# Optimization experiments

Hardware: AMD Instinct MI355X
Metric: run time of the kernel (lower is better)

The kernel has to match this reference:

```python
import jax, jax.numpy as jnp
import numpy as np

TWO_PI = 2.0 * np.pi

def ringify(x):
    # wrap values to [-pi, pi)
    return (x + np.pi) % TWO_PI - np.pi

def complex_mean(x, axes):
    # circular mean direction: atan2(sum sin, sum ringify(cos))
    dir_x = ringify(jnp.cos(x)).sum(axis=axes)
    dir_y = jnp.sin(x).sum(axis=axes)
    return jnp.arctan2(dir_y, dir_x)

def setup_inputs() -> dict:
    key = jax.random.key(0)
    k1, k2, k3, k4 = jax.random.split(key, 4)
    B = 4096
    return {
        "x": jax.random.normal(k1, (B, 1, 28, 28), dtype=jnp.float32),
        "conv1_w": jax.random.normal(k2, (4, 1, 2, 2), dtype=jnp.float32),
        "conv2_w": jax.random.normal(k3, (8, 4, 4, 4), dtype=jnp.float32),
        "ff_w": jax.random.normal(k4, (288, 10), dtype=jnp.float32),
    }

def reference(x, conv1_w, conv2_w, ff_w):
    B = x.shape[0]
    x = ringify(x).reshape(B, 1, 28, 28)

    # --- ring conv1: 2x2 kernel, stride 2 (non-overlapping patches) ---
    # [B,1,28,28] -> [B,14,14,1,2,2]  (matches unfold(2,2,2).unfold(3,2,2).permute)
    p1 = x.reshape(B, 1, 14, 2, 14, 2).transpose(0, 2, 4, 1, 3, 5)
    w1 = conv1_w.transpose(1, 2, 3, 0)            # [1,2,2,4]
    d1 = ringify(p1[..., None] - w1)              # [B,14,14,1,2,2,4]
    h1 = complex_mean(d1, (3, 4, 5))              # [B,14,14,4]

    # --- ring conv2: 4x4 kernel, stride 2 (overlapping patches) ---
    h1 = h1.transpose(0, 3, 1, 2)                 # [B,4,14,14]
    idx = (jnp.arange(6) * 2)[:, None] + jnp.arange(4)[None, :]  # [6,4] window rows/cols
    p2 = h1[:, :, idx, :][:, :, :, :, idx]        # [B,4,6,4,6,4]
    p2 = p2.transpose(0, 2, 4, 1, 3, 5)           # [B,6,6,4,4,4]
    w2 = conv2_w.transpose(1, 2, 3, 0)            # [4,4,4,8]
    d2 = ringify(p2[..., None] - w2)              # [B,6,6,4,4,4,8]
    h2 = complex_mean(d2, (3, 4, 5))              # [B,6,6,8]

    # --- ring feed-forward ---
    f = h2.reshape(B, 288)
    d3 = ringify(f[:, :, None] - ff_w)            # [B,288,10]
    out = complex_mean(d3, (1,))                  # [B,10]
    return jnp.sin(out)
```

## Files before the change

### kernel.cpp

```cpp
#include <hip/hip_runtime.h>
#include <math.h>

#define FFT_OFF 0
#define W2_OFF 2880
#define W1_OFF 3400

__global__ void precompute_trig(const float* __restrict__ w1,
                                const float* __restrict__ w2,
                                const float* __restrict__ ff,
                                float2* __restrict__ ws) {
    int idx = blockIdx.x * blockDim.x + threadIdx.x;
    if (idx < 2880) {
        int k = idx / 10, n = idx % 10;
        float s, c; sincosf(ff[idx], &s, &c);
        ws[FFT_OFF + n * 288 + k] = make_float2(c, s);
    } else if (idx < 3392) {
        int i = idx - 2880;
        int oc = i >> 6, e = i & 63;
        float s, c; sincosf(w2[i], &s, &c);
        ws[W2_OFF + (oc >> 1) * 130 + e * 2 + (oc & 1)] = make_float2(c, s);
    } else if (idx < 3408) {
        int i = idx - 3392;
        float s, c; sincosf(w1[i], &s, &c);
        ws[W1_OFF + i] = make_float2(c, s);
    }
}

__device__ __forceinline__ void conv1_pos(float2 r0, float2 r1,
                                          const float2* __restrict__ w1t,
                                          float2* __restrict__ sc1,
                                          int pi, int pj) {
    float sx[4], cx[4];
    __sincosf(r0.x, &sx[0], &cx[0]);
    __sincosf(r0.y, &sx[1], &cx[1]);
    __sincosf(r1.x, &sx[2], &cx[2]);
    __sincosf(r1.y, &sx[3], &cx[3]);
    #pragma unroll
    for (int oc = 0; oc < 4; oc++) {
        float4 wa = *(const float4*)(w1t + oc * 4);
        float4 wb = *(const float4*)(w1t + oc * 4 + 2);
        float Y = 0.f, X = 0.f;
        Y = fmaf(sx[0], wa.x, fmaf(-cx[0], wa.y, Y));
        X = fmaf(cx[0], wa.x, fmaf( sx[0], wa.y, X));
        Y = fmaf(sx[1], wa.z, fmaf(-cx[1], wa.w, Y));
        X = fmaf(cx[1], wa.z, fmaf( sx[1], wa.w, X));
        Y = fmaf(sx[2], wb.x, fmaf(-cx[2], wb.y, Y));
        X = fmaf(cx[2], wb.x, fmaf( sx[2], wb.y, X));
        Y = fmaf(sx[3], wb.z, fmaf(-cx[3], wb.w, Y));
        X = fmaf(cx[3], wb.z, fmaf( sx[3], wb.w, X));
        float inv = rsqrtf(fmaxf(fmaf(X, X, Y * Y), 1e-30f));
        sc1[oc * 252 + pi * 18 + pj] = make_float2(Y * inv, X * inv);
    }
}

__global__ __launch_bounds__(256, 4) void ringnn_kernel(
    const float* __restrict__ x,
    const float2* __restrict__ ws,
    float* __restrict__ out)
{
    __shared__ __align__(16) float2 trig2[520];
    __shared__ __align__(16) float2 sc1[2 * 1008];
    __shared__ __align__(16) float2 sc2[2 * 288];
    const int tid = threadIdx.x;
    const float2* __restrict__ fft = ws + FFT_OFF;
    const float2* __restrict__ w1t = ws + W1_OFF;
    const size_t img0 = (size_t)blockIdx.x * 2;

    const int im0 = (tid >= 196) ? 1 : 0;
    const int p0  = tid - im0 * 196;
    const int pi0 = p0 / 14, pj0 = p0 % 14;
    const float* xb0 = x + (img0 + im0) * 784;
    float2 a0 = *(const float2*)(xb0 + (2 * pi0) * 28 + 2 * pj0);
    float2 a1 = *(const float2*)(xb0 + (2 * pi0 + 1) * 28 + 2 * pj0);
    int pi1 = 0, pj1 = 0;
    float2 b0 = make_float2(0.f, 0.f), b1 = make_float2(0.f, 0.f);
    if (tid < 136) {
        int p = tid + 60;
        pi1 = p / 14; pj1 = p % 14;
        const float* xb1 = x + (img0 + 1) * 784;
        b0 = *(const float2*)(xb1 + (2 * pi1) * 28 + 2 * pj1);
        b1 = *(const float2*)(xb1 + (2 * pi1 + 1) * 28 + 2 * pj1);
    }

    for (int i = tid; i < 260; i += 256)
        ((float4*)trig2)[i] = ((const float4*)(ws + W2_OFF))[i];

    conv1_pos(a0, a1, w1t, sc1 + im0 * 1008, pi0, pj0);
    if (tid < 136) conv1_pos(b0, b1, w1t, sc1 + 1008, pi1, pj1);
    __syncthreads();

    if (tid < 192) {
        const int img = (tid >= 96) ? 1 : 0;
        int r = tid - img * 96;
        int oi = r >> 4, ojg = (r >> 3) & 1, ocp = (r >> 1) & 3, hf = r & 1;
        const float2* wbp = trig2 + ocp * 130;
        const float2* s1p = sc1 + img * 1008;
        float aY[3][2] = {{0.f,0.f},{0.f,0.f},{0.f,0.f}};
        float aX[3][2] = {{0.f,0.f},{0.f,0.f},{0.f,0.f}};
        #pragma unroll
        for (int ch = 0; ch < 4; ch++) {
            #pragma unroll
            for (int kk = 0; kk < 2; kk++) {
                int ki = hf * 2 + kk;
                int base = ch * 252 + (oi * 2 + ki) * 18 + ojg * 6;
                float4 f0 = *(const float4*)(s1p + base);
                float4 f1 = *(const float4*)(s1p + base + 2);
                float4 f2 = *(const float4*)(s1p + base + 4);
                float4 f3 = *(const float4*)(s1p + base + 6);
                float ss[8] = {f0.x,f0.z,f1.x,f1.z,f2.x,f2.z,f3.x,f3.z};
                float cc[8] = {f0.y,f0.w,f1.y,f1.w,f2.y,f2.w,f3.y,f3.w};
                int e0 = ch * 16 + ki * 4;
                #pragma unroll
                for (int kj = 0; kj < 4; kj++) {
                    float4 wv = *(const float4*)(wbp + (e0 + kj) * 2);
                    #pragma unroll
                    for (int ojl = 0; ojl < 3; ojl++) {
                        float s = ss[ojl * 2 + kj], c = cc[ojl * 2 + kj];
                        aY[ojl][0] = fmaf(s, wv.x, fmaf(-c, wv.y, aY[ojl][0]));
                        aX[ojl][0] = fmaf(c, wv.x, fmaf( s, wv.y, aX[ojl][0]));
                        aY[ojl][1] = fmaf(s, wv.z, fmaf(-c, wv.w, aY[ojl][1]));
                        aX[ojl][1] = fmaf(c, wv.z, fmaf( s, wv.w, aX[ojl][1]));
                    }
                }
            }
        }
        #pragma unroll
        for (int ojl = 0; ojl < 3; ojl++) {
            float y0 = aY[ojl][0]; y0 += __shfl_xor(y0, 1);
            float y1 = aY[ojl][1]; y1 += __shfl_xor(y1, 1);
            float x0 = aX[ojl][0]; x0 += __shfl_xor(x0, 1);
            float x1 = aX[ojl][1]; x1 += __shfl_xor(x1, 1);
            float Y = hf ? y1 : y0;
            float X = hf ? x1 : x0;
            float inv = rsqrtf(fmaxf(fmaf(X, X, Y * Y), 1e-30f));
            int p = oi * 6 + ojg * 3 + ojl;
            sc2[img * 288 + p * 8 + ocp * 2 + hf] = make_float2(Y * inv, X * inv);
        }
    }
    __syncthreads();

    #pragma unroll
    for (int rr = 0; rr < 3; rr++) {
        int t = tid + (rr << 8);
        if (t < 640) {
            int img = (t >= 320) ? 1 : 0;
            int idx = t - img * 320;
            int n = idx >> 5, s = idx & 31;
            const float2* wn = fft + n * 288;
            const float2* s2p = sc2 + img * 288;
            float Y = 0.f, X = 0.f;
            #pragma unroll
            for (int i = 0; i < 9; i++) {
                int k = i * 32 + s;
                float2 sc = s2p[k];
                float2 w = wn[k];
                Y = fmaf(sc.x, w.x, fmaf(-sc.y, w.y, Y));
                X = fmaf(sc.y, w.x, fmaf( sc.x, w.y, X));
            }
            #pragma unroll
            for (int off = 16; off > 0; off >>= 1) {
                Y += __shfl_down(Y, off, 32);
                X += __shfl_down(X, off, 32);
            }
            if (s == 0) {
                out[(img0 + img) * 10 + n] =
                    Y * rsqrtf(fmaxf(fmaf(X, X, Y * Y), 1e-30f));
            }
        }
    }
}

extern "C" void kernel_launch(void* const* d_in, const int* in_sizes, int n_in,
                              void* d_out, int out_size, void* d_ws, size_t ws_size,
                              hipStream_t stream) {
    const float* x  = (const float*)d_in[0];
    const float* w1 = (const float*)d_in[1];
    const float* w2 = (const float*)d_in[2];
    const float* ff = (const float*)d_in[3];
    float* out = (float*)d_out;
    const int B = in_sizes[0] / 784;

    float2* ws = (float2*)d_ws;
    precompute_trig<<<14, 256, 0, stream>>>(w1, w2, ff, ws);
    ringnn_kernel<<<B / 2, 256, 0, stream>>>(x, ws, out);
}
```

Baseline: 82.39 us.

## Process two image pairs per block with prefetch of second pair's input

Each block now handles four images as two sequential pairs, with the grid halved. The second pair's input pixels are loaded into registers before the feed-forward phase of the first pair, so global load latency overlaps compute. The shared conv2 weight load is also amortized over twice as many images. In exchange there are half as many blocks, so latency hiding across blocks is lower, and the extra live registers may add pressure.

Measured after the change: 82.10 us. No clear change (-0.3%).

```diff
diff --git a/kernel.cpp b/kernel.cpp
--- a/kernel.cpp
+++ b/kernel.cpp
@@ -64,110 +64,129 @@
     const int tid = threadIdx.x;
     const float2* __restrict__ fft = ws + FFT_OFF;
     const float2* __restrict__ w1t = ws + W1_OFF;
-    const size_t img0 = (size_t)blockIdx.x * 2;
+    const size_t imgBase = (size_t)blockIdx.x * 4;
 
     const int im0 = (tid >= 196) ? 1 : 0;
     const int p0  = tid - im0 * 196;
     const int pi0 = p0 / 14, pj0 = p0 % 14;
-    const float* xb0 = x + (img0 + im0) * 784;
-    float2 a0 = *(const float2*)(xb0 + (2 * pi0) * 28 + 2 * pj0);
-    float2 a1 = *(const float2*)(xb0 + (2 * pi0 + 1) * 28 + 2 * pj0);
-    int pi1 = 0, pj1 = 0;
-    float2 b0 = make_float2(0.f, 0.f), b1 = make_float2(0.f, 0.f);
-    if (tid < 136) {
-        int p = tid + 60;
-        pi1 = p / 14; pj1 = p % 14;
-        const float* xb1 = x + (img0 + 1) * 784;
-        b0 = *(const float2*)(xb1 + (2 * pi1) * 28 + 2 * pj1);
-        b1 = *(const float2*)(xb1 + (2 * pi1 + 1) * 28 + 2 * pj1);
-    }
-
+    const int pr1 = tid + 60;
+    const int pi1 = pr1 / 14, pj1 = pr1 % 14;
+
+    float2 a0, a1, b0 = make_float2(0.f, 0.f), b1 = make_float2(0.f, 0.f);
+
+    auto loadPair = [&](size_t pairImg) {
+        const float* xb0 = x + (pairImg + im0) * 784;
+        a0 = *(const float2*)(xb0 + (2 * pi0) * 28 + 2 * pj0);
+        a1 = *(const float2*)(xb0 + (2 * pi0 + 1) * 28 + 2 * pj0);
+        if (tid < 136) {
+            const float* xb1 = x + (pairImg + 1) * 784;
+            b0 = *(const float2*)(xb1 + (2 * pi1) * 28 + 2 * pj1);
+            b1 = *(const float2*)(xb1 + (2 * pi1 + 1) * 28 + 2 * pj1);
+        }
+    };
+
+    auto phase1 = [&]() {
+        conv1_pos(a0, a1, w1t, sc1 + im0 * 1008, pi0, pj0);
+        if (tid < 136) conv1_pos(b0, b1, w1t, sc1 + 1008, pi1, pj1);
+    };
+
+    auto phase2 = [&]() {
+        if (tid < 192) {
+            const int img = (tid >= 96) ? 1 : 0;
+            int r = tid - img * 96;
+            int oi = r >> 4, ojg = (r >> 3) & 1, ocp = (r >> 1) & 3, hf = r & 1;
+            const float2* wbp = trig2 + ocp * 130;
+            const float2* s1p = sc1 + img * 1008;
+            float aY[3][2] = {{0.f,0.f},{0.f,0.f},{0.f,0.f}};
+            float aX[3][2] = {{0.f,0.f},{0.f,0.f},{0.f,0.f}};
+            #pragma unroll
+            for (int ch = 0; ch < 4; ch++) {
+                #pragma unroll
+                for (int kk = 0; kk < 2; kk++) {
+                    int ki = hf * 2 + kk;
+                    int base = ch * 252 + (oi * 2 + ki) * 18 + ojg * 6;
+                    float4 f0 = *(const float4*)(s1p + base);
+                    float4 f1 = *(const float4*)(s1p + base + 2);
+                    float4 f2 = *(const float4*)(s1p + base + 4);
+                    float4 f3 = *(const float4*)(s1p + base + 6);
+                    float ss[8] = {f0.x,f0.z,f1.x,f1.z,f2.x,f2.z,f3.x,f3.z};
+                    float cc[8] = {f0.y,f0.w,f1.y,f1.w,f2.y,f2.w,f3.y,f3.w};
+                    int e0 = ch * 16 + ki * 4;
+                    #pragma unroll
+                    for (int kj = 0; kj < 4; kj++) {
+                        float4 wv = *(const float4*)(wbp + (e0 + kj) * 2);
+                        #pragma unroll
+                        for (int ojl = 0; ojl < 3; ojl++) {
+                            float s = ss[ojl * 2 + kj], c = cc[ojl * 2 + kj];
+                            aY[ojl][0] = fmaf(s, wv.x, fmaf(-c, wv.y, aY[ojl][0]));
+                            aX[ojl][0] = fmaf(c, wv.x, fmaf( s, wv.y, aX[ojl][0]));
+                            aY[ojl][1] = fmaf(s, wv.z, fmaf(-c, wv.w, aY[ojl][1]));
+                            aX[ojl][1] = fmaf(c, wv.z, fmaf( s, wv.w, aX[ojl][1]));
+                        }
+                    }
+                }
+            }
+            #pragma unroll
+            for (int ojl = 0; ojl < 3; ojl++) {
+                float y0 = aY[ojl][0]; y0 += __shfl_xor(y0, 1);
+                float y1 = aY[ojl][1]; y1 += __shfl_xor(y1, 1);
+                float x0 = aX[ojl][0]; x0 += __shfl_xor(x0, 1);
+                float x1 = aX[ojl][1]; x1 += __shfl_xor(x1, 1);
+                float Y = hf ? y1 : y0;
+                float X = hf ? x1 : x0;
+                float inv = rsqrtf(fmaxf(fmaf(X, X, Y * Y), 1e-30f));
+                int p = oi * 6 + ojg * 3 + ojl;
+                sc2[img * 288 + p * 8 + ocp * 2 + hf] = make_float2(Y * inv, X * inv);
+            }
+        }
+    };
+
+    auto phase3 = [&](size_t pairImg) {
+        #pragma unroll
+        for (int rr = 0; rr < 3; rr++) {
+            int t = tid + (rr << 8);
+            if (t < 640) {
+                int img = (t >= 320) ? 1 : 0;
+                int idx = t - img * 320;
+                int n = idx >> 5, s = idx & 31;
+                const float2* wn = fft + n * 288;
+                const float2* s2p = sc2 + img * 288;
+                float Y = 0.f, X = 0.f;
+                #pragma unroll
+                for (int i = 0; i < 9; i++) {
+                    int k = i * 32 + s;
+                    float2 sc = s2p[k];
+                    float2 w = wn[k];
+                    Y = fmaf(sc.x, w.x, fmaf(-sc.y, w.y, Y));
+                    X = fmaf(sc.y, w.x, fmaf( sc.x, w.y, X));
+                }
+                #pragma unroll
+                for (int off = 16; off > 0; off >>= 1) {
+                    Y += __shfl_down(Y, off, 32);
+                    X += __shfl_down(X, off, 32);
+                }
+                if (s == 0) {
+                    out[(pairImg + img) * 10 + n] =
+                        Y * rsqrtf(fmaxf(fmaf(X, X, Y * Y), 1e-30f));
+                }
+            }
+        }
+    };
+
+    loadPair(imgBase);
     for (int i = tid; i < 260; i += 256)
         ((float4*)trig2)[i] = ((const float4*)(ws + W2_OFF))[i];
-
-    conv1_pos(a0, a1, w1t, sc1 + im0 * 1008, pi0, pj0);
-    if (tid < 136) conv1_pos(b0, b1, w1t, sc1 + 1008, pi1, pj1);
-    __syncthreads();
-
-    if (tid < 192) {
-        const int img = (tid >= 96) ? 1 : 0;
-        int r = tid - img * 96;
-        int oi = r >> 4, ojg = (r >> 3) & 1, ocp = (r >> 1) & 3, hf = r & 1;
-        const float2* wbp = trig2 + ocp * 130;
-        const float2* s1p = sc1 + img * 1008;
-        float aY[3][2] = {{0.f,0.f},{0.f,0.f},{0.f,0.f}};
-        float aX[3][2] = {{0.f,0.f},{0.f,0.f},{0.f,0.f}};
-        #pragma unroll
-        for (int ch = 0; ch < 4; ch++) {
-            #pragma unroll
-            for (int kk = 0; kk < 2; kk++) {
-                int ki = hf * 2 + kk;
-                int base = ch * 252 + (oi * 2 + ki) * 18 + ojg * 6;
-                float4 f0 = *(const float4*)(s1p + base);
-                float4 f1 = *(const float4*)(s1p + base + 2);
-                float4 f2 = *(const float4*)(s1p + base + 4);
-                float4 f3 = *(const float4*)(s1p + base + 6);
-                float ss[8] = {f0.x,f0.z,f1.x,f1.z,f2.x,f2.z,f3.x,f3.z};
-                float cc[8] = {f0.y,f0.w,f1.y,f1.w,f2.y,f2.w,f3.y,f3.w};
-                int e0 = ch * 16 + ki * 4;
-                #pragma unroll
-                for (int kj = 0; kj < 4; kj++) {
-                    float4 wv = *(const float4*)(wbp + (e0 + kj) * 2);
-                    #pragma unroll
-                    for (int ojl = 0; ojl < 3; ojl++) {
-                        float s = ss[ojl * 2 + kj], c = cc[ojl * 2 + kj];
-                        aY[ojl][0] = fmaf(s, wv.x, fmaf(-c, wv.y, aY[ojl][0]));
-                        aX[ojl][0] = fmaf(c, wv.x, fmaf( s, wv.y, aX[ojl][0]));
-                        aY[ojl][1] = fmaf(s, wv.z, fmaf(-c, wv.w, aY[ojl][1]));
-                        aX[ojl][1] = fmaf(c, wv.z, fmaf( s, wv.w, aX[ojl][1]));
-                    }
-                }
-            }
-        }
-        #pragma unroll
-        for (int ojl = 0; ojl < 3; ojl++) {
-            float y0 = aY[ojl][0]; y0 += __shfl_xor(y0, 1);
-            float y1 = aY[ojl][1]; y1 += __shfl_xor(y1, 1);
-            float x0 = aX[ojl][0]; x0 += __shfl_xor(x0, 1);
-            float x1 = aX[ojl][1]; x1 += __shfl_xor(x1, 1);
-            float Y = hf ? y1 : y0;
-            float X = hf ? x1 : x0;
-            float inv = rsqrtf(fmaxf(fmaf(X, X, Y * Y), 1e-30f));
-            int p = oi * 6 + ojg * 3 + ojl;
-            sc2[img * 288 + p * 8 + ocp * 2 + hf] = make_float2(Y * inv, X * inv);
-        }
-    }
-    __syncthreads();
-
-    #pragma unroll
-    for (int rr = 0; rr < 3; rr++) {
-        int t = tid + (rr << 8);
-        if (t < 640) {
-            int img = (t >= 320) ? 1 : 0;
-            int idx = t - img * 320;
-            int n = idx >> 5, s = idx & 31;
-            const float2* wn = fft + n * 288;
-            const float2* s2p = sc2 + img * 288;
-            float Y = 0.f, X = 0.f;
-            #pragma unroll
-            for (int i = 0; i < 9; i++) {
-                int k = i * 32 + s;
-                float2 sc = s2p[k];
-                float2 w = wn[k];
-                Y = fmaf(sc.x, w.x, fmaf(-sc.y, w.y, Y));
-                X = fmaf(sc.y, w.x, fmaf( sc.x, w.y, X));
-            }
-            #pragma unroll
-            for (int off = 16; off > 0; off >>= 1) {
-                Y += __shfl_down(Y, off, 32);
-                X += __shfl_down(X, off, 32);
-            }
-            if (s == 0) {
-                out[(img0 + img) * 10 + n] =
-                    Y * rsqrtf(fmaxf(fmaf(X, X, Y * Y), 1e-30f));
-            }
-        }
-    }
+    phase1();
+    __syncthreads();
+    phase2();
+    __syncthreads();
+    loadPair(imgBase + 2);
+    phase3(imgBase);
+    phase1();
+    __syncthreads();
+    phase2();
+    __syncthreads();
+    phase3(imgBase + 2);
 }
 
 extern "C" void kernel_launch(void* const* d_in, const int* in_sizes, int n_in,
@@ -182,5 +201,5 @@
 
     float2* ws = (float2*)d_ws;
     precompute_trig<<<14, 256, 0, stream>>>(w1, w2, ff, ws);
-    ringnn_kernel<<<B / 2, 256, 0, stream>>>(x, ws, out);
-}
+    ringnn_kernel<<<B / 4, 256, 0, stream>>>(x, ws, out);
+}
```
